# Kernel tuning notes

Measured on AMD Instinct MI355X. Metric: run time of the kernel, lower is better.

## Reference

```python
import jax, jax.numpy as jnp
import numpy as np

BETA = 0.25
EPS = 1e-12


def l2_normalize(x, axis=-1, eps=EPS):
    return x * jax.lax.rsqrt((x * x).sum(axis=axis, keepdims=True) + eps)


def setup_inputs() -> dict:
    key = jax.random.key(0)
    k1, k2 = jax.random.split(key)
    z = jax.random.normal(k1, (16, 32, 32, 256), dtype=jnp.float32)
    # embedding_init = uniform(2.0, -1.0) -> U[-1, 1)
    embedding = jax.random.uniform(k2, (8192, 256), dtype=jnp.float32) * 2.0 - 1.0
    return {"z": z, "embedding": embedding}


def reference(z, embedding):
    e_dim = embedding.shape[-1]
    z_flat = jnp.reshape(z, (-1, e_dim))                      # [N, D]
    z_flat_n = l2_normalize(z_flat, axis=-1)                  # [N, D]
    emb_n = l2_normalize(embedding, axis=-1)                  # [K, D]
    # squared L2 distance between normalized vectors
    d = (jnp.sum(z_flat_n ** 2, axis=1, keepdims=True)
         + jnp.sum(emb_n ** 2, axis=1)
         - 2.0 * jnp.einsum('nd,kd->nk', z_flat_n, emb_n))    # [N, K]
    min_idx = jnp.reshape(jnp.argmin(d, axis=1), z.shape[:-1])  # [B,H,W]
    # codebook lookup + renormalize
    z_q = l2_normalize(jnp.take(embedding, min_idx, axis=0), axis=-1)  # [B,H,W,D]
    z_norm = l2_normalize(z, axis=-1)
    loss = (BETA * jnp.mean(jnp.square(jax.lax.stop_gradient(z_q) - z_norm))
            + jnp.mean(jnp.square(z_q - jax.lax.stop_gradient(z_norm))))
    # straight-through estimator
    z_q_st = z + jax.lax.stop_gradient(z_q - z)
    return (z_q_st, loss, min_idx)
```

## Files before the change

kernel.cpp:

```cpp
#include <hip/hip_runtime.h>
#include <math.h>

#define D 256
#define NROW 16384
#define KCODE 8192
#define MARGIN 1.2e-3f

typedef _Float16 half8 __attribute__((ext_vector_type(8)));
typedef _Float16 half4f __attribute__((ext_vector_type(4)));
typedef __attribute__((ext_vector_type(4))) float f32x4;

__device__ __forceinline__ float dot4(float4 a, float4 b) {
  return a.x * b.x + a.y * b.y + a.z * b.z + a.w * b.w;
}
__device__ __forceinline__ float wave_sum(float s) {
#pragma unroll
  for (int off = 32; off; off >>= 1) s += __shfl_xor(s, off, 64);
  return s;
}
__device__ __forceinline__ float wave_min_f(float v) {
#pragma unroll
  for (int off = 32; off; off >>= 1) v = fminf(v, __shfl_xor(v, off, 64));
  return v;
}
__device__ __forceinline__ void async16(const void* g, void* l) {
  __builtin_amdgcn_global_load_lds(
      (const __attribute__((address_space(1))) unsigned int*)g,
      (__attribute__((address_space(3))) unsigned int*)l, 16, 0, 0);
}

__global__ __launch_bounds__(256) void k_prep(const float* __restrict__ emb,
                                              const float* __restrict__ z,
                                              float* __restrict__ emb_n,
                                              float* __restrict__ e2,
                                              _Float16* __restrict__ Bb,
                                              _Float16* __restrict__ Ab) {
  const int b = blockIdx.x;
  const int w = threadIdx.x >> 6, l = threadIdx.x & 63;
  if (b < 2048) {
    int row = b * 4 + w;
    float4 v = ((const float4*)(emb + (size_t)row * D))[l];
    float s = wave_sum(dot4(v, v));
    float inv = 1.0f / sqrtf(s + 1e-12f);
    v.x *= inv; v.y *= inv; v.z *= inv; v.w *= inv;
    ((float4*)(emb_n + (size_t)row * D))[l] = v;
    float s2 = wave_sum(dot4(v, v));
    if (l == 0) e2[row] = s2;
    half4f h;
    h[0] = (_Float16)v.x; h[1] = (_Float16)v.y;
    h[2] = (_Float16)v.z; h[3] = (_Float16)v.w;
    *(half4f*)(Bb + (size_t)row * 256 + 4 * l) = h;
  } else {
    int row = (b - 2048) * 4 + w;
    float4 v = ((const float4*)(z + (size_t)row * D))[l];
    float s = wave_sum(dot4(v, v));
    float inv = 1.0f / sqrtf(s + 1e-12f);
    v.x *= inv; v.y *= inv; v.z *= inv; v.w *= inv;
    half4f h;
    h[0] = (_Float16)v.x; h[1] = (_Float16)v.y;
    h[2] = (_Float16)v.z; h[3] = (_Float16)v.w;
    *(half4f*)(Ab + (size_t)row * 256 + 4 * l) = h;
  }
}

__device__ __forceinline__ void merge2(float& d1, int& k1, float& d2, int& k2,
                                       float od1, int ok1, float od2, int ok2) {
  bool w1 = (od1 < d1) || (od1 == d1 && ok1 < k1);
  float n1 = w1 ? od1 : d1; int nk1 = w1 ? ok1 : k1;
  float c  = w1 ? d1 : od1; int ck  = w1 ? k1 : ok1;
  float c2 = w1 ? od2 : d2; int ck2 = w1 ? ok2 : k2;
  bool w2 = (c2 < c) || (c2 == c && ck2 < ck);
  d1 = n1; k1 = nk1;
  d2 = w2 ? c2 : c; k2 = w2 ? ck2 : ck;
}

__global__ __launch_bounds__(256, 4) void k_gemm_argmin6(
    const _Float16* __restrict__ Cb,
    const _Float16* __restrict__ Zb,
    const float* __restrict__ e2, float4* __restrict__ top2) {
  __shared__ _Float16 As[128 * 64];
  __shared__ _Float16 Bs[128 * 64];
  const int tid = threadIdx.x, w = tid >> 6, l = tid & 63;
  const int wm = w >> 1, wn = w & 1;
  const int quad = l >> 4, col = l & 15;
  const int xcd = blockIdx.x & 7;
  const int j = blockIdx.x >> 3;
  const int ct = xcd * 8 + (j & 7);
  const int zt = j >> 3;
  const int c0 = ct * 128;
  const size_t z0 = (size_t)zt * 128;

  const int srow = tid >> 3, su = tid & 7;
  const int g = su ^ (srow & 7);
  const _Float16* gA = Cb + ((size_t)c0 + srow) * 256 + g * 8;
  const _Float16* gB = Zb + (z0 + srow) * 256 + g * 8;
  char* dA = (char*)As + srow * 128 + su * 16;
  char* dB = (char*)Bs + srow * 128 + su * 16;

  f32x4 acc[4][4] = {};
  const int ub = col & 7;

  for (int s = 0; s < 4; ++s) {
    const int k0 = s * 64;
#pragma unroll
    for (int p = 0; p < 4; ++p) {
      async16(gA + (size_t)p * 32 * 256 + k0, dA + p * 4096);
      async16(gB + (size_t)p * 32 * 256 + k0, dB + p * 4096);
    }
    __syncthreads();
#pragma unroll
    for (int par = 0; par < 2; ++par) {
      const int uoff = (((par * 4 + quad) ^ ub) << 4);
      half8 af[4], bf[4];
#pragma unroll
      for (int mf = 0; mf < 4; ++mf)
        af[mf] = *(const half8*)((const char*)As + (wm * 64 + mf * 16 + col) * 128 + uoff);
#pragma unroll
      for (int nf = 0; nf < 4; ++nf)
        bf[nf] = *(const half8*)((const char*)Bs + (wn * 64 + nf * 16 + col) * 128 + uoff);
#pragma unroll
      for (int mf = 0; mf < 4; ++mf)
#pragma unroll
        for (int nf = 0; nf < 4; ++nf)
          acc[mf][nf] = __builtin_amdgcn_mfma_f32_16x16x32_f16(af[mf], bf[nf], acc[mf][nf], 0, 0, 0);
    }
    __syncthreads();
  }

  float e2r[16];
#pragma unroll
  for (int mf = 0; mf < 4; ++mf)
#pragma unroll
    for (int v = 0; v < 4; ++v)
      e2r[mf * 4 + v] = e2[c0 + wm * 64 + mf * 16 + quad * 4 + v];

  float4* mbuf = (float4*)As;
#pragma unroll
  for (int nf = 0; nf < 4; ++nf) {
    float d1 = 1e30f, d2 = 1e30f; int k1 = 0, k2 = 0;
#pragma unroll
    for (int mf = 0; mf < 4; ++mf)
#pragma unroll
      for (int v = 0; v < 4; ++v) {
        float d = fmaf(-2.0f, acc[mf][nf][v], e2r[mf * 4 + v]);
        int kc = c0 + wm * 64 + mf * 16 + quad * 4 + v;
        bool lt1 = d < d1, lt2 = d < d2;
        d2 = lt1 ? d1 : (lt2 ? d : d2);
        k2 = lt1 ? k1 : (lt2 ? kc : k2);
        d1 = lt1 ? d : d1;
        k1 = lt1 ? kc : k1;
      }
#pragma unroll
    for (int m = 16; m < 64; m <<= 1) {
      float od1 = __shfl_xor(d1, m, 64); int ok1 = __shfl_xor(k1, m, 64);
      float od2 = __shfl_xor(d2, m, 64); int ok2 = __shfl_xor(k2, m, 64);
      merge2(d1, k1, d2, k2, od1, ok1, od2, ok2);
    }
    if (quad == 0)
      mbuf[(wm * 2 + wn) * 64 + nf * 16 + col] =
          make_float4(d1, d2, __int_as_float(k1), __int_as_float(k2));
  }
  __syncthreads();
  if (tid < 128) {
    const int wnn = tid >> 6, zc = tid & 63;
    float4 a = mbuf[(0 * 2 + wnn) * 64 + zc];
    float4 b = mbuf[(1 * 2 + wnn) * 64 + zc];
    float d1 = a.x, d2 = a.y; int k1 = __float_as_int(a.z), k2 = __float_as_int(a.w);
    merge2(d1, k1, d2, k2, b.x, __float_as_int(b.z), b.y, __float_as_int(b.w));
    top2[((size_t)zt * 64 + ct) * 128 + tid] =
        make_float4(d1, d2, __int_as_float(k1), __int_as_float(k2));
  }
}

__global__ __launch_bounds__(256) void k_refine_gather(
    const float* __restrict__ z, const float* __restrict__ emb_n,
    const float* __restrict__ e2, const float4* __restrict__ top2,
    float* __restrict__ out0, float* __restrict__ idx_out,
    float* __restrict__ lsum, int* __restrict__ wl_row,
    unsigned long long* __restrict__ wl_mask, double* __restrict__ wl_best,
    int* __restrict__ wl_bk, int* __restrict__ n_flag) {
  __shared__ float zr[4][D];
  __shared__ float4 t2s[4][64];
  const int t = threadIdx.x;
  const int w = t >> 6, l = t & 63;
  const int row = blockIdx.x * 4 + w;
  float4 zv = ((const float4*)(z + (size_t)row * D))[l];
  float s = wave_sum(dot4(zv, zv));
  float inv = 1.0f / sqrtf(s + 1e-12f);
  float4 zn = make_float4(zv.x * inv, zv.y * inv, zv.z * inv, zv.w * inv);
  ((float4*)zr[w])[l] = zn;
  {
    const int zt = (blockIdx.x * 4) >> 7;
    const int rb = (blockIdx.x * 4) & 127;
    t2s[t & 3][t >> 2] = top2[((size_t)zt * 64 + (t >> 2)) * 128 + rb + (t & 3)];
  }
  __syncthreads();

  float4 e = t2s[w][l];
  const float ad1 = e.x, ad2 = e.y;
  const int ck1 = __float_as_int(e.z), ck2 = __float_as_int(e.w);
  const float d1g = wave_min_f(ad1);
  const float win = d1g + 2.0f * MARGIN;

  double best = 1e300; int bk = 0x7fffffff;
  unsigned long long m1 = __ballot(ad1 <= win);
  unsigned long long m2 = __ballot(ad2 <= win);
#pragma unroll 1
  for (int slot = 0; slot < 2; ++slot) {
    unsigned long long mm = slot ? m2 : m1;
    while (mm) {
      int ln = __builtin_ctzll(mm); mm &= mm - 1;
      int k = __shfl(slot ? ck2 : ck1, ln, 64);
      float4 e4 = ((const float4*)(emb_n + (size_t)k * D))[l];
      float4 z4 = ((const float4*)zr[w])[l];
      double p = (double)e4.x * (double)z4.x + (double)e4.y * (double)z4.y +
                 (double)e4.z * (double)z4.z + (double)e4.w * (double)z4.w;
#pragma unroll
      for (int off = 32; off; off >>= 1) p += __shfl_xor(p, off, 64);
      double dd = (double)e2[k] - 2.0 * p;
      if (dd < best || (dd == best && k < bk)) { best = dd; bk = k; }
    }
  }
  float4 q = ((const float4*)(emb_n + (size_t)bk * D))[l];
  float4 o;
  o.x = zv.x + (q.x - zv.x); o.y = zv.y + (q.y - zv.y);
  o.z = zv.z + (q.z - zv.z); o.w = zv.w + (q.w - zv.w);
  ((float4*)(out0 + (size_t)row * D))[l] = o;
  float dx = q.x - zn.x, dy = q.y - zn.y, dz = q.z - zn.z, dw = q.w - zn.w;
  float lp = wave_sum(dx * dx + dy * dy + dz * dz + dw * dw);
  if (l == 0) {
    lsum[row] = lp;
    idx_out[row] = (float)bk;
    if (m2) {
      int p = atomicAdd(n_flag, 1);
      wl_row[p] = row; wl_mask[p] = m2; wl_best[p] = best; wl_bk[p] = bk;
    }
  }
}

__global__ __launch_bounds__(256) void k_rescan(
    const float* __restrict__ z, const float* __restrict__ emb_n,
    const float* __restrict__ e2, const int* __restrict__ wl_row,
    const unsigned long long* __restrict__ wl_mask,
    const double* __restrict__ wl_best, const int* __restrict__ wl_bk,
    const int* __restrict__ n_flag, float* __restrict__ idx_out,
    float* __restrict__ out0, float* __restrict__ lsum) {
  __shared__ float zr[D];
  __shared__ double ph[128];
  __shared__ double sd[4];
  __shared__ int si[4];
  __shared__ int s_bk;
  const int tid = threadIdx.x;
  const int nf = *n_flag;
  for (int wi = blockIdx.x; wi < nf; wi += gridDim.x) {
    const int row = wl_row[wi];
    unsigned long long mask = wl_mask[wi];
    __syncthreads();
    if (tid < 64) {
      float4 zv = ((const float4*)(z + (size_t)row * D))[tid];
      float s = wave_sum(dot4(zv, zv));
      float inv = 1.0f / sqrtf(s + 1e-12f);
      ((float4*)zr)[tid] = make_float4(zv.x * inv, zv.y * inv, zv.z * inv, zv.w * inv);
    }
    __syncthreads();
    double best = wl_best[wi]; int bk = wl_bk[wi];
    while (mask) {
      const int sl = __builtin_ctzll(mask); mask &= mask - 1;
      const int code = (sl << 7) + (tid & 127);
      const int half = tid >> 7;
      const float4* ev = (const float4*)(emb_n + (size_t)code * D) + half * 32;
      const float4* zf = ((const float4*)zr) + half * 32;
      double a0 = 0.0, a1 = 0.0;
#pragma unroll 8
      for (int i = 0; i < 32; i += 2) {
        float4 e0 = ev[i], e1 = ev[i + 1], z0 = zf[i], z1 = zf[i + 1];
        a0 += (double)e0.x * (double)z0.x + (double)e0.y * (double)z0.y +
              (double)e0.z * (double)z0.z + (double)e0.w * (double)z0.w;
        a1 += (double)e1.x * (double)z1.x + (double)e1.y * (double)z1.y +
              (double)e1.z * (double)z1.z + (double)e1.w * (double)z1.w;
      }
      double p = a0 + a1;
      if (half) ph[tid & 127] = p;
      __syncthreads();
      if (!half) {
        double dd = (double)e2[code] - 2.0 * (p + ph[tid]);
        if (dd < best || (dd == best && code < bk)) { best = dd; bk = code; }
      }
      __syncthreads();
    }
#pragma unroll
    for (int off = 32; off; off >>= 1) {
      double od = __shfl_xor(best, off, 64); int ok = __shfl_xor(bk, off, 64);
      if (od < best || (od == best && ok < bk)) { best = od; bk = ok; }
    }
    if ((tid & 63) == 0) { sd[tid >> 6] = best; si[tid >> 6] = bk; }
    __syncthreads();
    if (tid == 0) {
#pragma unroll
      for (int q = 1; q < 4; ++q)
        if (sd[q] < best || (sd[q] == best && si[q] < bk)) { best = sd[q]; bk = si[q]; }
      s_bk = bk;
      idx_out[row] = (float)bk;
    }
    __syncthreads();
    const int fk = s_bk;
    if (tid < 64) {
      float4 zv = ((const float4*)(z + (size_t)row * D))[tid];
      float4 zn = ((const float4*)zr)[tid];
      float4 q = ((const float4*)(emb_n + (size_t)fk * D))[tid];
      float4 o;
      o.x = zv.x + (q.x - zv.x); o.y = zv.y + (q.y - zv.y);
      o.z = zv.z + (q.z - zv.z); o.w = zv.w + (q.w - zv.w);
      ((float4*)(out0 + (size_t)row * D))[tid] = o;
      float dx = q.x - zn.x, dy = q.y - zn.y, dz = q.z - zn.z, dw = q.w - zn.w;
      float lp = wave_sum(dx * dx + dy * dy + dz * dz + dw * dw);
      if (tid == 0) lsum[row] = lp;
    }
  }
}

__global__ __launch_bounds__(256) void k_reduce(const float* __restrict__ lsum,
                                                float* __restrict__ loss_out,
                                                float inv_cnt) {
  __shared__ float ws4[4];
  float s = 0.0f;
  const float4* p = (const float4*)lsum;
  for (int i = threadIdx.x; i < NROW / 4; i += 256) {
    float4 v = p[i];
    s += (v.x + v.y) + (v.z + v.w);
  }
  s = wave_sum(s);
  if ((threadIdx.x & 63) == 0) ws4[threadIdx.x >> 6] = s;
  __syncthreads();
  if (threadIdx.x == 0) {
    float m = ((ws4[0] + ws4[1]) + (ws4[2] + ws4[3])) * inv_cnt;
    *loss_out = 0.25f * m + m;
  }
}

__device__ __forceinline__ int sw_f(int row, int d4) { return row * D + 4 * (d4 ^ (row & 7)); }
__global__ __launch_bounds__(256, 1) void k_argmin_f32(const float* __restrict__ z,
                                                       const float* __restrict__ emb_n,
                                                       const float* __restrict__ e2,
                                                       float* __restrict__ idx_out, int K) {
  extern __shared__ float smem[];
  float* zs = smem; float* es = smem + 64 * D;
  int tid = threadIdx.x; int w = tid >> 6, l = tid & 63;
  size_t r0 = (size_t)blockIdx.x * 64;
#pragma unroll
  for (int i = 0; i < 16; ++i) {
    int row = 4 * i + w;
    float4 v = ((const float4*)(z + (r0 + row) * D))[l];
    float s = wave_sum(dot4(v, v));
    float inv = 1.0f / sqrtf(s + 1e-12f);
    v.x *= inv; v.y *= inv; v.z *= inv; v.w *= inv;
    *(float4*)(&zs[sw_f(row, l)]) = v;
  }
  __syncthreads();
  int tc = tid & 15, tr = tid >> 4;
  float bestd[4] = {1e30f, 1e30f, 1e30f, 1e30f};
  int bestk[4] = {0, 0, 0, 0};
  for (int k0 = 0; k0 < K; k0 += 64) {
#pragma unroll
    for (int i = 0; i < 16; ++i) {
      int row = 4 * i + w;
      float4 v = ((const float4*)(emb_n + (size_t)(k0 + row) * D))[l];
      *(float4*)(&es[sw_f(row, l)]) = v;
    }
    __syncthreads();
    float acc[4][4] = {};
#pragma unroll 4
    for (int d4 = 0; d4 < 64; ++d4) {
      float4 zv[4], ev[4];
#pragma unroll
      for (int i = 0; i < 4; ++i) zv[i] = *(const float4*)(&zs[sw_f(tr + 16 * i, d4)]);
#pragma unroll
      for (int jx = 0; jx < 4; ++jx) ev[jx] = *(const float4*)(&es[sw_f(tc + 16 * jx, d4)]);
#pragma unroll
      for (int i = 0; i < 4; ++i)
#pragma unroll
        for (int jx = 0; jx < 4; ++jx)
          acc[i][jx] = fmaf(zv[i].x, ev[jx].x, fmaf(zv[i].y, ev[jx].y,
                       fmaf(zv[i].z, ev[jx].z, fmaf(zv[i].w, ev[jx].w, acc[i][jx]))));
    }
#pragma unroll
    for (int jx = 0; jx < 4; ++jx) {
      int k = k0 + tc + 16 * jx;
      float ek = e2[k];
#pragma unroll
      for (int i = 0; i < 4; ++i) {
        float dd = fmaf(-2.0f, acc[i][jx], ek);
        if (dd < bestd[i]) { bestd[i] = dd; bestk[i] = k; }
      }
    }
    __syncthreads();
  }
#pragma unroll
  for (int i = 0; i < 4; ++i) {
    float dd = bestd[i]; int kkk = bestk[i];
#pragma unroll
    for (int off = 1; off < 16; off <<= 1) {
      float od = __shfl_xor(dd, off, 64); int ok = __shfl_xor(kkk, off, 64);
      if (od < dd || (od == dd && ok < kkk)) { dd = od; kkk = ok; }
    }
    if (tc == 0) idx_out[r0 + tr + 16 * i] = (float)kkk;
  }
}

__global__ __launch_bounds__(256) void k_gather(const float* __restrict__ z,
                                                const float* __restrict__ emb_n,
                                                const float* __restrict__ idx_f,
                                                float* __restrict__ out0,
                                                float* __restrict__ loss_acc) {
  __shared__ float wsum[4];
  int w = threadIdx.x >> 6, l = threadIdx.x & 63;
  int row = blockIdx.x * 4 + w;
  float4 zv = ((const float4*)(z + (size_t)row * D))[l];
  float s = wave_sum(dot4(zv, zv));
  float inv = 1.0f / sqrtf(s + 1e-12f);
  int k = (int)idx_f[row];
  float4 q = ((const float4*)(emb_n + (size_t)k * D))[l];
  float4 o;
  o.x = zv.x + (q.x - zv.x); o.y = zv.y + (q.y - zv.y);
  o.z = zv.z + (q.z - zv.z); o.w = zv.w + (q.w - zv.w);
  ((float4*)(out0 + (size_t)row * D))[l] = o;
  float dx = q.x - zv.x * inv, dy = q.y - zv.y * inv;
  float dz = q.z - zv.z * inv, dw = q.w - zv.w * inv;
  float lp = wave_sum(dx * dx + dy * dy + dz * dz + dw * dw);
  if (l == 0) wsum[w] = lp;
  __syncthreads();
  if (threadIdx.x == 0) atomicAdd(loss_acc, wsum[0] + wsum[1] + wsum[2] + wsum[3]);
}

__global__ void k_final(const float* __restrict__ loss_acc,
                        float* __restrict__ loss_out, float inv_cnt) {
  float m = *loss_acc * inv_cnt;
  *loss_out = 0.25f * m + m;
}

extern "C" void kernel_launch(void* const* d_in, const int* in_sizes, int n_in,
                              void* d_out, int out_size, void* d_ws, size_t ws_size,
                              hipStream_t stream) {
  const float* z = (const float*)d_in[0];
  const float* emb = (const float*)d_in[1];
  int N = in_sizes[0] / D;
  int K = in_sizes[1] / D;

  float* out0 = (float*)d_out;
  float* loss_out = out0 + (size_t)N * D;
  float* idx_out = loss_out + 1;

  char* ws = (char*)d_ws;
  float* emb_n = (float*)ws;
  float* e2 = (float*)(ws + 8388608);
  float* loss_acc = (float*)(ws + 8421376);
  int* n_flag = (int*)(ws + 8421380);
  float* lsum = (float*)(ws + 8421392);
  _Float16* Bb = (_Float16*)(ws + 8486928);
  _Float16* Ab = (_Float16*)(ws + 12681232);
  float4* top2 = (float4*)(ws + 21069840);
  const size_t NEED = 37847056;
  int* wl_row = (int*)Ab;
  unsigned long long* wl_mask = (unsigned long long*)((char*)Ab + 65536);
  double* wl_best = (double*)((char*)Ab + 196608);
  int* wl_bk = (int*)((char*)Ab + 327680);

  const float inv_cnt = 1.0f / (float)((size_t)N * D);
  hipMemsetAsync(loss_acc, 0, 8, stream);
  if (ws_size >= NEED) {
    k_prep<<<K / 4 + N / 4, 256, 0, stream>>>(emb, z, emb_n, e2, Bb, Ab);
    k_gemm_argmin6<<<(K / 128) * (N / 128), 256, 0, stream>>>(Bb, Ab, e2, top2);
    k_refine_gather<<<N / 4, 256, 0, stream>>>(z, emb_n, e2, top2, out0, idx_out,
                                               lsum, wl_row, wl_mask, wl_best,
                                               wl_bk, n_flag);
    k_rescan<<<1024, 256, 0, stream>>>(z, emb_n, e2, wl_row, wl_mask, wl_best,
                                       wl_bk, n_flag, idx_out, out0, lsum);
    k_reduce<<<1, 256, 0, stream>>>(lsum, loss_out, inv_cnt);
  } else {
    k_prep<<<K / 4 + N / 4, 256, 0, stream>>>(emb, z, emb_n, e2, Bb, Ab);
    k_argmin_f32<<<N / 64, 256, 131072, stream>>>(z, emb_n, e2, idx_out, K);
    k_gather<<<N / 4, 256, 0, stream>>>(z, emb_n, idx_out, out0, loss_acc);
    k_final<<<1, 1, 0, stream>>>(loss_acc, loss_out, inv_cnt);
  }
}
```

Baseline: 210.3 us.

## Double-buffer LDS tiles in GEMM-argmin kernel to overlap loads with MFMA

The fp16 GEMM-argmin kernel now keeps two LDS stages for each operand. It prefetches the next 64-wide K slice asynchronously while MFMAs run on the current slice, which replaces two barriers per stage with one wait and one barrier. It also raises wave priority around the MFMA block and hoists the e2 loads ahead of the main loop. In exchange, LDS per block doubles and the launch bound drops to 2 blocks per CU, which reduces occupancy.

```diff
diff --git a/kernel.cpp b/kernel.cpp
--- a/kernel.cpp
+++ b/kernel.cpp
@@ -74,12 +74,12 @@
   d2 = w2 ? c2 : c; k2 = w2 ? ck2 : ck;
 }
 
-__global__ __launch_bounds__(256, 4) void k_gemm_argmin6(
+__global__ __launch_bounds__(256, 2) void k_gemm_argmin7(
     const _Float16* __restrict__ Cb,
     const _Float16* __restrict__ Zb,
     const float* __restrict__ e2, float4* __restrict__ top2) {
-  __shared__ _Float16 As[128 * 64];
-  __shared__ _Float16 Bs[128 * 64];
+  __shared__ _Float16 As[2 * 128 * 64];
+  __shared__ _Float16 Bs[2 * 128 * 64];
   const int tid = threadIdx.x, w = tid >> 6, l = tid & 63;
   const int wm = w >> 1, wn = w & 1;
   const int quad = l >> 4, col = l & 15;
@@ -100,39 +100,58 @@
   f32x4 acc[4][4] = {};
   const int ub = col & 7;
 
+  float e2r[16];
+#pragma unroll
+  for (int mf = 0; mf < 4; ++mf)
+#pragma unroll
+    for (int v = 0; v < 4; ++v)
+      e2r[mf * 4 + v] = e2[c0 + wm * 64 + mf * 16 + quad * 4 + v];
+
+#pragma unroll
+  for (int p = 0; p < 4; ++p) {
+    async16(gA + (size_t)p * 32 * 256, dA + p * 4096);
+    async16(gB + (size_t)p * 32 * 256, dB + p * 4096);
+  }
+  asm volatile("s_waitcnt vmcnt(0)" ::: "memory");
+  __builtin_amdgcn_s_barrier();
+  __builtin_amdgcn_sched_barrier(0);
+
+#pragma unroll
   for (int s = 0; s < 4; ++s) {
-    const int k0 = s * 64;
-#pragma unroll
-    for (int p = 0; p < 4; ++p) {
-      async16(gA + (size_t)p * 32 * 256 + k0, dA + p * 4096);
-      async16(gB + (size_t)p * 32 * 256 + k0, dB + p * 4096);
-    }
-    __syncthreads();
+    const int cur = (s & 1) * 16384;
+    if (s < 3) {
+      const int nxt = ((s + 1) & 1) * 16384;
+      const int k0 = (s + 1) * 64;
+#pragma unroll
+      for (int p = 0; p < 4; ++p) {
+        async16(gA + (size_t)p * 32 * 256 + k0, dA + nxt + p * 4096);
+        async16(gB + (size_t)p * 32 * 256 + k0, dB + nxt + p * 4096);
+      }
+    }
 #pragma unroll
     for (int par = 0; par < 2; ++par) {
       const int uoff = (((par * 4 + quad) ^ ub) << 4);
       half8 af[4], bf[4];
 #pragma unroll
       for (int mf = 0; mf < 4; ++mf)
-        af[mf] = *(const half8*)((const char*)As + (wm * 64 + mf * 16 + col) * 128 + uoff);
+        af[mf] = *(const half8*)((const char*)As + cur + (wm * 64 + mf * 16 + col) * 128 + uoff);
 #pragma unroll
       for (int nf = 0; nf < 4; ++nf)
-        bf[nf] = *(const half8*)((const char*)Bs + (wn * 64 + nf * 16 + col) * 128 + uoff);
+        bf[nf] = *(const half8*)((const char*)Bs + cur + (wn * 64 + nf * 16 + col) * 128 + uoff);
+      __builtin_amdgcn_s_setprio(1);
 #pragma unroll
       for (int mf = 0; mf < 4; ++mf)
 #pragma unroll
         for (int nf = 0; nf < 4; ++nf)
           acc[mf][nf] = __builtin_amdgcn_mfma_f32_16x16x32_f16(af[mf], bf[nf], acc[mf][nf], 0, 0, 0);
-    }
-    __syncthreads();
-  }
-
-  float e2r[16];
-#pragma unroll
-  for (int mf = 0; mf < 4; ++mf)
-#pragma unroll
-    for (int v = 0; v < 4; ++v)
-      e2r[mf * 4 + v] = e2[c0 + wm * 64 + mf * 16 + quad * 4 + v];
+      __builtin_amdgcn_s_setprio(0);
+    }
+    if (s < 3) {
+      asm volatile("s_waitcnt vmcnt(0)" ::: "memory");
+      __builtin_amdgcn_s_barrier();
+      __builtin_amdgcn_sched_barrier(0);
+    }
+  }
 
   float4* mbuf = (float4*)As;
 #pragma unroll
@@ -469,7 +488,7 @@
   hipMemsetAsync(loss_acc, 0, 8, stream);
   if (ws_size >= NEED) {
     k_prep<<<K / 4 + N / 4, 256, 0, stream>>>(emb, z, emb_n, e2, Bb, Ab);
-    k_gemm_argmin6<<<(K / 128) * (N / 128), 256, 0, stream>>>(Bb, Ab, e2, top2);
+    k_gemm_argmin7<<<(K / 128) * (N / 128), 256, 0, stream>>>(Bb, Ab, e2, top2);
     k_refine_gather<<<N / 4, 256, 0, stream>>>(z, emb_n, e2, top2, out0, idx_out,
                                                lsum, wl_row, wl_mask, wl_best,
                                                wl_bk, n_flag);
```

Measured after the change: 232.5 us. +10.5%, slower.

## Pre-tile fp16 operands into MFMA fragment layout and load GEMM operands directly to registers

Applied to the files above, without the earlier changes.

The prep kernel now writes the normalized fp16 codebook and inputs in a tiled layout that matches the MFMA 16x16x32 fragment order, arranged per 128-row tile and per 32-wide k phase. The GEMM+argmin kernel drops LDS staging and its barriers. Each wave reads its fragments straight from global memory into registers, with a two-phase register double buffer and s_setprio around the MFMA bursts. Occupancy is lowered to 3 blocks per CU. The goal is to remove LDS round-trips and __syncthreads stalls. In exchange, operands shared between waves are fetched redundantly through the cache, and register pressure rises.

```diff
diff --git a/kernel.cpp b/kernel.cpp
--- a/kernel.cpp
+++ b/kernel.cpp
@@ -22,11 +22,6 @@
 #pragma unroll
   for (int off = 32; off; off >>= 1) v = fminf(v, __shfl_xor(v, off, 64));
   return v;
-}
-__device__ __forceinline__ void async16(const void* g, void* l) {
-  __builtin_amdgcn_global_load_lds(
-      (const __attribute__((address_space(1))) unsigned int*)g,
-      (__attribute__((address_space(3))) unsigned int*)l, 16, 0, 0);
 }
 
 __global__ __launch_bounds__(256) void k_prep(const float* __restrict__ emb,
@@ -37,6 +32,9 @@
                                               _Float16* __restrict__ Ab) {
   const int b = blockIdx.x;
   const int w = threadIdx.x >> 6, l = threadIdx.x & 63;
+  const int ph = l >> 3;
+  const int qd = (l & 7) >> 1;
+  const int hf = l & 1;
   if (b < 2048) {
     int row = b * 4 + w;
     float4 v = ((const float4*)(emb + (size_t)row * D))[l];
@@ -49,7 +47,10 @@
     half4f h;
     h[0] = (_Float16)v.x; h[1] = (_Float16)v.y;
     h[2] = (_Float16)v.z; h[3] = (_Float16)v.w;
-    *(half4f*)(Bb + (size_t)row * 256 + 4 * l) = h;
+    int t = row >> 7, r = row & 127;
+    size_t off = (size_t)t * 32768 + ph * 4096 + (r >> 6) * 2048 +
+                 ((r >> 4) & 3) * 512 + (qd * 16 + (r & 15)) * 8 + hf * 4;
+    *(half4f*)(Bb + off) = h;
   } else {
     int row = (b - 2048) * 4 + w;
     float4 v = ((const float4*)(z + (size_t)row * D))[l];
@@ -59,7 +60,10 @@
     half4f h;
     h[0] = (_Float16)v.x; h[1] = (_Float16)v.y;
     h[2] = (_Float16)v.z; h[3] = (_Float16)v.w;
-    *(half4f*)(Ab + (size_t)row * 256 + 4 * l) = h;
+    int t = row >> 7, r = row & 127;
+    size_t off = (size_t)t * 32768 + ph * 4096 + (r >> 6) * 2048 +
+                 ((r >> 4) & 3) * 512 + (qd * 16 + (r & 15)) * 8 + hf * 4;
+    *(half4f*)(Ab + off) = h;
   }
 }
 
@@ -74,12 +78,11 @@
   d2 = w2 ? c2 : c; k2 = w2 ? ck2 : ck;
 }
 
-__global__ __launch_bounds__(256, 4) void k_gemm_argmin6(
+__global__ __launch_bounds__(256, 3) void k_gemm_argmin10(
     const _Float16* __restrict__ Cb,
     const _Float16* __restrict__ Zb,
     const float* __restrict__ e2, float4* __restrict__ top2) {
-  __shared__ _Float16 As[128 * 64];
-  __shared__ _Float16 Bs[128 * 64];
+  __shared__ float4 mbuf[256];
   const int tid = threadIdx.x, w = tid >> 6, l = tid & 63;
   const int wm = w >> 1, wn = w & 1;
   const int quad = l >> 4, col = l & 15;
@@ -88,43 +91,45 @@
   const int ct = xcd * 8 + (j & 7);
   const int zt = j >> 3;
   const int c0 = ct * 128;
-  const size_t z0 = (size_t)zt * 128;
-
-  const int srow = tid >> 3, su = tid & 7;
-  const int g = su ^ (srow & 7);
-  const _Float16* gA = Cb + ((size_t)c0 + srow) * 256 + g * 8;
-  const _Float16* gB = Zb + (z0 + srow) * 256 + g * 8;
-  char* dA = (char*)As + srow * 128 + su * 16;
-  char* dB = (char*)Bs + srow * 128 + su * 16;
+
+  const _Float16* At = Cb + (size_t)ct * 32768 + wm * 2048 + l * 8;
+  const _Float16* Bt = Zb + (size_t)zt * 32768 + wn * 2048 + l * 8;
 
   f32x4 acc[4][4] = {};
-  const int ub = col & 7;
-
-  for (int s = 0; s < 4; ++s) {
-    const int k0 = s * 64;
-#pragma unroll
-    for (int p = 0; p < 4; ++p) {
-      async16(gA + (size_t)p * 32 * 256 + k0, dA + p * 4096);
-      async16(gB + (size_t)p * 32 * 256 + k0, dB + p * 4096);
-    }
-    __syncthreads();
-#pragma unroll
-    for (int par = 0; par < 2; ++par) {
-      const int uoff = (((par * 4 + quad) ^ ub) << 4);
-      half8 af[4], bf[4];
-#pragma unroll
-      for (int mf = 0; mf < 4; ++mf)
-        af[mf] = *(const half8*)((const char*)As + (wm * 64 + mf * 16 + col) * 128 + uoff);
+  half8 a0[4], b0[4], a1[4], b1[4];
+#pragma unroll
+  for (int mf = 0; mf < 4; ++mf) {
+    a0[mf] = *(const half8*)(At + mf * 512);
+    b0[mf] = *(const half8*)(Bt + mf * 512);
+  }
+#pragma unroll
+  for (int ph = 0; ph < 8; ph += 2) {
+#pragma unroll
+    for (int mf = 0; mf < 4; ++mf) {
+      a1[mf] = *(const half8*)(At + (ph + 1) * 4096 + mf * 512);
+      b1[mf] = *(const half8*)(Bt + (ph + 1) * 4096 + mf * 512);
+    }
+    __builtin_amdgcn_s_setprio(1);
+#pragma unroll
+    for (int mf = 0; mf < 4; ++mf)
 #pragma unroll
       for (int nf = 0; nf < 4; ++nf)
-        bf[nf] = *(const half8*)((const char*)Bs + (wn * 64 + nf * 16 + col) * 128 + uoff);
-#pragma unroll
-      for (int mf = 0; mf < 4; ++mf)
-#pragma unroll
-        for (int nf = 0; nf < 4; ++nf)
-          acc[mf][nf] = __builtin_amdgcn_mfma_f32_16x16x32_f16(af[mf], bf[nf], acc[mf][nf], 0, 0, 0);
-    }
-    __syncthreads();
+        acc[mf][nf] = __builtin_amdgcn_mfma_f32_16x16x32_f16(a0[mf], b0[nf], acc[mf][nf], 0, 0, 0);
+    __builtin_amdgcn_s_setprio(0);
+    if (ph < 6) {
+#pragma unroll
+      for (int mf = 0; mf < 4; ++mf) {
+        a0[mf] = *(const half8*)(At + (ph + 2) * 4096 + mf * 512);
+        b0[mf] = *(const half8*)(Bt + (ph + 2) * 4096 + mf * 512);
+      }
+    }
+    __builtin_amdgcn_s_setprio(1);
+#pragma unroll
+    for (int mf = 0; mf < 4; ++mf)
+#pragma unroll
+      for (int nf = 0; nf < 4; ++nf)
+        acc[mf][nf] = __builtin_amdgcn_mfma_f32_16x16x32_f16(a1[mf], b1[nf], acc[mf][nf], 0, 0, 0);
+    __builtin_amdgcn_s_setprio(0);
   }
 
   float e2r[16];
@@ -134,7 +139,6 @@
     for (int v = 0; v < 4; ++v)
       e2r[mf * 4 + v] = e2[c0 + wm * 64 + mf * 16 + quad * 4 + v];
 
-  float4* mbuf = (float4*)As;
 #pragma unroll
   for (int nf = 0; nf < 4; ++nf) {
     float d1 = 1e30f, d2 = 1e30f; int k1 = 0, k2 = 0;
@@ -469,7 +473,7 @@
   hipMemsetAsync(loss_acc, 0, 8, stream);
   if (ws_size >= NEED) {
     k_prep<<<K / 4 + N / 4, 256, 0, stream>>>(emb, z, emb_n, e2, Bb, Ab);
-    k_gemm_argmin6<<<(K / 128) * (N / 128), 256, 0, stream>>>(Bb, Ab, e2, top2);
+    k_gemm_argmin10<<<(K / 128) * (N / 128), 256, 0, stream>>>(Bb, Ab, e2, top2);
     k_refine_gather<<<N / 4, 256, 0, stream>>>(z, emb_n, e2, top2, out0, idx_out,
                                                lsum, wl_row, wl_mask, wl_best,
                                                wl_bk, n_flag);
```

After: 198.8 us. -5.5%, faster.
